# Kernel tuning notes

Measured on AMD Instinct MI355X. Metric: run time of the kernel, lower is better.

## Reference

```python
import jax, jax.numpy as jnp
import numpy as np

B, C, H, W = 16, 256, 128, 128
RED = 16  # reduction -> hidden = C // RED = 16


def setup_inputs() -> dict:
    key = jax.random.key(0)
    k = jax.random.split(key, 5)
    hid = C // RED
    return {
        "x": jax.random.normal(k[0], (B, C, H, W), dtype=jnp.float32),
        "w1": jax.random.normal(k[1], (hid, C), dtype=jnp.float32) * 0.05,
        "b1": jax.random.normal(k[2], (hid,), dtype=jnp.float32) * 0.05,
        "w2": jax.random.normal(k[3], (C, hid), dtype=jnp.float32) * 0.05,
        "b2": jax.random.normal(k[4], (C,), dtype=jnp.float32) * 0.05,
    }


def reference(x, w1, b1, w2, b2):
    # Global average pool over H, W -> [B, C]
    y = jnp.mean(x, axis=(2, 3))
    # 2-layer MLP (nn.Linear: y @ W.T + b) + sigmoid -> per-channel gates [B, C]
    h = jax.nn.relu(y @ w1.T + b1)
    s = jax.nn.sigmoid(h @ w2.T + b2)
    # Faithful to the original loop: only batch element 0 gets scaled by s[0].
    return x.at[0].multiply(s[0][:, None, None])
```

## Files before the change

kernel.cpp:

```cpp
#include <hip/hip_runtime.h>
#include <math.h>

#define HW    16384
#define CCH   256
#define HID   16

__global__ void se_pool(const float* __restrict__ x, float* __restrict__ y) {
    const int c = blockIdx.x;
    const float4* p = (const float4*)(x + (size_t)c * HW);
    float sum = 0.f;
    for (int i = threadIdx.x; i < HW / 4; i += blockDim.x) {
        float4 v = p[i];
        sum += (v.x + v.y) + (v.z + v.w);
    }
    #pragma unroll
    for (int off = 32; off > 0; off >>= 1)
        sum += __shfl_down(sum, off, 64);
    __shared__ float wsum[4];
    const int lane = threadIdx.x & 63;
    const int wave = threadIdx.x >> 6;
    if (lane == 0) wsum[wave] = sum;
    __syncthreads();
    if (threadIdx.x == 0) {
        float s = (wsum[0] + wsum[1]) + (wsum[2] + wsum[3]);
        y[c] = s * (1.0f / (float)HW);
    }
}

__global__ void se_mlp(const float* __restrict__ y,
                       const float* __restrict__ w1, const float* __restrict__ b1,
                       const float* __restrict__ w2, const float* __restrict__ b2,
                       float* __restrict__ s) {
    __shared__ float ysh[CCH];
    __shared__ float h[HID];
    const int t = threadIdx.x;
    ysh[t] = y[t];
    __syncthreads();
    if (t < HID) {
        float acc = b1[t];
        const float* wr = w1 + t * CCH;
        #pragma unroll 8
        for (int c = 0; c < CCH; ++c) acc = fmaf(ysh[c], wr[c], acc);
        h[t] = fmaxf(acc, 0.f);
    }
    __syncthreads();
    float acc = b2[t];
    const float* wr2 = w2 + t * HID;
    #pragma unroll
    for (int j = 0; j < HID; ++j) acc = fmaf(h[j], wr2[j], acc);
    s[t] = 1.0f / (1.0f + __expf(-acc));
}

__global__ void se_scale(const float* __restrict__ x, const float* __restrict__ s,
                         float* __restrict__ out) {
    const float4* __restrict__ xin = (const float4*)x;
    float4* __restrict__ o = (float4*)out;
    const size_t n4 = (size_t)16 * CCH * (HW / 4);
    const size_t b0 = (size_t)CCH * (HW / 4);
    size_t i = (size_t)blockIdx.x * blockDim.x + threadIdx.x;
    const size_t stride = (size_t)gridDim.x * blockDim.x;
    for (; i < n4; i += stride) {
        float4 v = xin[i];
        if (i < b0) {
            const float g = s[i >> 12];
            v.x *= g; v.y *= g; v.z *= g; v.w *= g;
        }
        o[i] = v;
    }
}

extern "C" void kernel_launch(void* const* d_in, const int* in_sizes, int n_in,
                              void* d_out, int out_size, void* d_ws, size_t ws_size,
                              hipStream_t stream) {
    const float* x  = (const float*)d_in[0];
    const float* w1 = (const float*)d_in[1];
    const float* b1 = (const float*)d_in[2];
    const float* w2 = (const float*)d_in[3];
    const float* b2 = (const float*)d_in[4];
    float* out = (float*)d_out;

    float* y = (float*)d_ws;
    float* s = y + CCH;

    se_pool<<<CCH, 256, 0, stream>>>(x, y);
    se_mlp<<<1, 256, 0, stream>>>(y, w1, b1, w2, b2, s);
    se_scale<<<16384, 256, 0, stream>>>(x, s, out);
}
```

Before: 449.5 us.

## Fuse pool, MLP and scale into one cooperative kernel with grid syncs

Replaces the three launches with one cooperative kernel. Each of 1024 blocks pools a quarter of one batch-0 channel and writes a partial sum. After a grid sync, block 0 runs the MLP while every block copies the unscaled batches 1-15. A second grid sync follows, then each block rescales its own batch-0 chunk, which is likely still in cache. This removes launch gaps and overlaps the serial MLP with the bulk copy, at the cost of two grid-wide barriers and a fixed grid size that must all be resident at once.

```diff
diff --git a/kernel.cpp b/kernel.cpp
--- a/kernel.cpp
+++ b/kernel.cpp
@@ -1,71 +1,81 @@
 #include <hip/hip_runtime.h>
+#include <hip/hip_cooperative_groups.h>
 #include <math.h>
 
-#define HW    16384
-#define CCH   256
-#define HID   16
+namespace cg = cooperative_groups;
 
-__global__ void se_pool(const float* __restrict__ x, float* __restrict__ y) {
-    const int c = blockIdx.x;
-    const float4* p = (const float4*)(x + (size_t)c * HW);
+#define HW       16384
+#define CCH      256
+#define HID      16
+#define NBLK     1024
+#define NTHR     256
+#define NTHREADS (NBLK * NTHR)
+#define B0_VEC   1048576
+#define TOT_VEC  16777216
+
+__launch_bounds__(NTHR, 4)
+__global__ void se_fused(const float* __restrict__ x,
+                         const float* __restrict__ w1, const float* __restrict__ b1,
+                         const float* __restrict__ w2, const float* __restrict__ b2,
+                         float* __restrict__ out, float* __restrict__ ws) {
+    const int t = threadIdx.x;
+    const int b = blockIdx.x;
+    const float4* __restrict__ x4 = (const float4*)x;
+    float4* __restrict__ o4 = (float4*)out;
+
+    __shared__ float wsum[4];
+    __shared__ float ysh[CCH];
+    __shared__ float h[HID];
+
+    const size_t chunk = (size_t)b * 1024;
     float sum = 0.f;
-    for (int i = threadIdx.x; i < HW / 4; i += blockDim.x) {
-        float4 v = p[i];
+    #pragma unroll
+    for (int k = 0; k < 4; ++k) {
+        float4 v = x4[chunk + (size_t)k * 256 + t];
         sum += (v.x + v.y) + (v.z + v.w);
     }
     #pragma unroll
     for (int off = 32; off > 0; off >>= 1)
         sum += __shfl_down(sum, off, 64);
-    __shared__ float wsum[4];
-    const int lane = threadIdx.x & 63;
-    const int wave = threadIdx.x >> 6;
-    if (lane == 0) wsum[wave] = sum;
+    if ((t & 63) == 0) wsum[t >> 6] = sum;
     __syncthreads();
-    if (threadIdx.x == 0) {
-        float s = (wsum[0] + wsum[1]) + (wsum[2] + wsum[3]);
-        y[c] = s * (1.0f / (float)HW);
+    if (t == 0) ws[b] = (wsum[0] + wsum[1]) + (wsum[2] + wsum[3]);
+
+    cg::this_grid().sync();
+
+    if (b == 0) {
+        float yv = (ws[4 * t] + ws[4 * t + 1] + ws[4 * t + 2] + ws[4 * t + 3])
+                   * (1.0f / (float)HW);
+        ysh[t] = yv;
+        __syncthreads();
+        if (t < HID) {
+            float acc = b1[t];
+            const float* wr = w1 + t * CCH;
+            #pragma unroll 8
+            for (int c = 0; c < CCH; ++c) acc = fmaf(ysh[c], wr[c], acc);
+            h[t] = fmaxf(acc, 0.f);
+        }
+        __syncthreads();
+        float acc = b2[t];
+        const float* wr2 = w2 + t * HID;
+        #pragma unroll
+        for (int j = 0; j < HID; ++j) acc = fmaf(h[j], wr2[j], acc);
+        ws[2048 + t] = 1.0f / (1.0f + __expf(-acc));
     }
-}
 
-__global__ void se_mlp(const float* __restrict__ y,
-                       const float* __restrict__ w1, const float* __restrict__ b1,
-                       const float* __restrict__ w2, const float* __restrict__ b2,
-                       float* __restrict__ s) {
-    __shared__ float ysh[CCH];
-    __shared__ float h[HID];
-    const int t = threadIdx.x;
-    ysh[t] = y[t];
-    __syncthreads();
-    if (t < HID) {
-        float acc = b1[t];
-        const float* wr = w1 + t * CCH;
-        #pragma unroll 8
-        for (int c = 0; c < CCH; ++c) acc = fmaf(ysh[c], wr[c], acc);
-        h[t] = fmaxf(acc, 0.f);
-    }
-    __syncthreads();
-    float acc = b2[t];
-    const float* wr2 = w2 + t * HID;
+    const int tid = b * NTHR + t;
+    for (size_t i = (size_t)B0_VEC + tid; i < TOT_VEC; i += NTHREADS)
+        o4[i] = x4[i];
+
+    cg::this_grid().sync();
+
+    const float g = ws[2048 + (b >> 2)];
     #pragma unroll
-    for (int j = 0; j < HID; ++j) acc = fmaf(h[j], wr2[j], acc);
-    s[t] = 1.0f / (1.0f + __expf(-acc));
-}
-
-__global__ void se_scale(const float* __restrict__ x, const float* __restrict__ s,
-                         float* __restrict__ out) {
-    const float4* __restrict__ xin = (const float4*)x;
-    float4* __restrict__ o = (float4*)out;
-    const size_t n4 = (size_t)16 * CCH * (HW / 4);
-    const size_t b0 = (size_t)CCH * (HW / 4);
-    size_t i = (size_t)blockIdx.x * blockDim.x + threadIdx.x;
-    const size_t stride = (size_t)gridDim.x * blockDim.x;
-    for (; i < n4; i += stride) {
-        float4 v = xin[i];
-        if (i < b0) {
-            const float g = s[i >> 12];
-            v.x *= g; v.y *= g; v.z *= g; v.w *= g;
-        }
-        o[i] = v;
+    for (int k = 0; k < 4; ++k) {
+        const size_t i = chunk + (size_t)k * 256 + t;
+        float4 v = x4[i];
+        v.x *= g; v.y *= g; v.z *= g; v.w *= g;
+        o4[i] = v;
     }
 }
 
@@ -78,11 +88,10 @@
     const float* w2 = (const float*)d_in[3];
     const float* b2 = (const float*)d_in[4];
     float* out = (float*)d_out;
+    float* ws  = (float*)d_ws;
 
-    float* y = (float*)d_ws;
-    float* s = y + CCH;
-
-    se_pool<<<CCH, 256, 0, stream>>>(x, y);
-    se_mlp<<<1, 256, 0, stream>>>(y, w1, b1, w2, b2, s);
-    se_scale<<<16384, 256, 0, stream>>>(x, s, out);
+    void* args[] = {(void*)&x, (void*)&w1, (void*)&b1, (void*)&w2, (void*)&b2,
+                    (void*)&out, (void*)&ws};
+    hipLaunchCooperativeKernel((void*)se_fused, dim3(NBLK), dim3(NTHR),
+                               args, 0, stream);
 }
```

Measured after the change: 637.5 us. 1.42x slower.
